# Optimization experiments

Hardware: AMD Instinct MI355X
Metric: run time of the kernel (lower is better)

## Reference

```python
import jax, jax.numpy as jnp
import numpy as np

H, DH = 12, 64
D = H * DH
EPS = 1e-5
NEG = -10000.0


def _layernorm(x, gamma, beta):
    mu = jnp.mean(x, axis=-1, keepdims=True)
    var = jnp.mean(jnp.square(x - mu), axis=-1, keepdims=True)
    return (x - mu) * jax.lax.rsqrt(var + EPS) * gamma + beta


def setup_inputs() -> dict:
    key = jax.random.key(0)
    ks = jax.random.split(key, 10)
    B, E, L = 1, 64, 256
    x = jax.random.normal(ks[0], (B, E, L, D), dtype=jnp.float32)
    padding_mask = jax.random.bernoulli(ks[1], 0.1, (B, E, L))
    s = 1.0 / np.sqrt(D)
    w_row = jax.random.normal(ks[2], (3 * D, D), dtype=jnp.float32) * s
    b_row = jnp.zeros((3 * D,), dtype=jnp.float32)
    w_col = jax.random.normal(ks[3], (3 * D, D), dtype=jnp.float32) * s
    b_col = jnp.zeros((3 * D,), dtype=jnp.float32)
    gamma1 = jnp.ones((D,), dtype=jnp.float32)
    beta1 = jnp.zeros((D,), dtype=jnp.float32)
    gamma2 = jnp.ones((D,), dtype=jnp.float32)
    beta2 = jnp.zeros((D,), dtype=jnp.float32)
    return {"x": x, "padding_mask": padding_mask, "w_row": w_row, "b_row": b_row,
            "w_col": w_col, "b_col": b_col, "gamma1": gamma1, "beta1": beta1,
            "gamma2": gamma2, "beta2": beta2}


def _qkv(x, w, b, B, E, L):
    qkv = x @ w.T + b  # [B,E,L,3D]
    q, k, v = jnp.split(qkv, 3, axis=-1)
    rs = lambda t: t.reshape(B, E, L, H, DH)
    return rs(q), rs(k), rs(v)


def reference(x, padding_mask, w_row, b_row, w_col, b_col, gamma1, beta1, gamma2, beta2):
    B, E, L, _ = x.shape
    mask = jnp.where(padding_mask, NEG, 0.0).astype(x.dtype)  # [B,E,L], same per head

    # ---- tied row attention ----
    q, k, v = _qkv(x, w_row, b_row, B, E, L)
    q = q * (DH * E) ** (-0.5)
    row_logits = jnp.einsum('bsihc,bsjhc->bhij', q, k)  # [B,H,L,L], tied over E
    row_logits = row_logits + mask.sum(axis=1)[:, None, None, :]  # sum over E, bcast over i,h
    row_maps = jax.nn.softmax(row_logits, axis=-1)
    row_out = jnp.einsum('bhij,bsjhc->bsihc', row_maps, v).reshape(B, E, L, D)
    out = _layernorm(x + row_out, gamma1, beta1)

    # ---- column attention ----
    q, k, v = _qkv(out, w_col, b_col, B, E, L)
    q = q * DH ** (-0.5)
    col_logits = jnp.einsum('bilhc,bjlhc->bhijl', q, k)  # [B,H,E,E,L]
    col_logits = col_logits + mask[:, None, None, :, :]  # bcast over h,i; applied along j
    col_maps = jax.nn.softmax(col_logits, axis=-2)
    col_out = jnp.einsum('bhijl,bjlhc->bilhc', col_maps, v).reshape(B, E, L, D)
    out = _layernorm(out + col_out, gamma2, beta2)

    return out, row_maps[:, :, None, :, :]  # row maps returned as [B,H,1,L,L]
```

## Files before the change

### kernel.cpp

```cpp
#include <hip/hip_runtime.h>
#include <hip/hip_bf16.h>
#include <float.h>

#define E_  64
#define L_  256
#define D_  768
#define H_  12
#define DH_ 64
#define TD_ 2304
#define NEGV -10000.0f
#define EPS_ 1e-5f

#define GM 16384
#define GN 2304
#define GK 768

#define RSPLIT 8

typedef __attribute__((ext_vector_type(8))) __bf16 bf16x8;
typedef __attribute__((ext_vector_type(4))) float f32x4;
typedef __attribute__((ext_vector_type(8))) unsigned short u16x8;

__device__ __forceinline__ float wred_sum64(float v){
  #pragma unroll
  for (int o = 32; o > 0; o >>= 1) v += __shfl_xor(v, o, 64);
  return v;
}
__device__ __forceinline__ float wred_max64(float v){
  #pragma unroll
  for (int o = 32; o > 0; o >>= 1) v = fmaxf(v, __shfl_xor(v, o, 64));
  return v;
}
__device__ __forceinline__ unsigned short f2bf(float f){
  unsigned int u = __float_as_uint(f);
  u += 0x7FFF + ((u >> 16) & 1);
  return (unsigned short)(u >> 16);
}
__device__ __forceinline__ float bf2f(unsigned short s){
  return __uint_as_float(((unsigned int)s) << 16);
}

__global__ __launch_bounds__(256) void f2b_kernel(
    const float* __restrict__ in, unsigned short* __restrict__ out){
  size_t i = ((size_t)blockIdx.x * 256 + threadIdx.x) * 8;
  float4 a = *(const float4*)(in + i);
  float4 b = *(const float4*)(in + i + 4);
  u16x8 o;
  o[0]=f2bf(a.x); o[1]=f2bf(a.y); o[2]=f2bf(a.z); o[3]=f2bf(a.w);
  o[4]=f2bf(b.x); o[5]=f2bf(b.y); o[6]=f2bf(b.z); o[7]=f2bf(b.w);
  *(u16x8*)(out + i) = o;
}

__global__ void masksum_kernel(const int* __restrict__ pm, float* __restrict__ msum){
  int l = threadIdx.x;
  int cnt = 0;
  #pragma unroll
  for (int s = 0; s < E_; ++s) cnt += (pm[s * L_ + l] != 0);
  msum[l] = NEGV * (float)cnt;
}

__global__ __launch_bounds__(256) void gemm_mfma_nt(
    const unsigned short* __restrict__ A,
    const unsigned short* __restrict__ W,
    const float* __restrict__ bias,
    unsigned short* __restrict__ C){
  __shared__ unsigned short As[128*32] __attribute__((aligned(16)));
  __shared__ unsigned short Bs[128*32] __attribute__((aligned(16)));
  int tid = threadIdx.x;
  int lane = tid & 63, wave = tid >> 6;
  int wr = wave >> 1, wc = wave & 1;
  int m0 = blockIdx.y * 128, n0 = blockIdx.x * 128;
  int col16 = lane & 15, kgrp = lane >> 4;

  f32x4 zero = {0.f, 0.f, 0.f, 0.f};
  f32x4 acc[4][4];
  #pragma unroll
  for (int mf = 0; mf < 4; ++mf)
    #pragma unroll
    for (int nf = 0; nf < 4; ++nf) acc[mf][nf] = zero;

  int srow = lane >> 2;
  int kchunk = (lane & 3) * 8;
  const unsigned short* Ag = A + (size_t)(m0 + wave * 32 + srow) * GK + kchunk;
  const unsigned short* Wg = W + (size_t)(n0 + wave * 32 + srow) * GK + kchunk;
  unsigned short* AsB = &As[(wave * 32) * 32];
  unsigned short* BsB = &Bs[(wave * 32) * 32];

  for (int k0 = 0; k0 < GK; k0 += 32) {
    __syncthreads();
    __builtin_amdgcn_global_load_lds(
      (const __attribute__((address_space(1))) unsigned int*)(Ag + k0),
      (__attribute__((address_space(3))) unsigned int*)(AsB), 16, 0, 0);
    __builtin_amdgcn_global_load_lds(
      (const __attribute__((address_space(1))) unsigned int*)(Ag + 16 * GK + k0),
      (__attribute__((address_space(3))) unsigned int*)(AsB + 16 * 32), 16, 0, 0);
    __builtin_amdgcn_global_load_lds(
      (const __attribute__((address_space(1))) unsigned int*)(Wg + k0),
      (__attribute__((address_space(3))) unsigned int*)(BsB), 16, 0, 0);
    __builtin_amdgcn_global_load_lds(
      (const __attribute__((address_space(1))) unsigned int*)(Wg + 16 * GK + k0),
      (__attribute__((address_space(3))) unsigned int*)(BsB + 16 * 32), 16, 0, 0);
    __syncthreads();
    bf16x8 af[4], bfr[4];
    #pragma unroll
    for (int mf = 0; mf < 4; ++mf)
      af[mf] = *(const bf16x8*)&As[(wr * 64 + mf * 16 + col16) * 32 + kgrp * 8];
    #pragma unroll
    for (int nf = 0; nf < 4; ++nf)
      bfr[nf] = *(const bf16x8*)&Bs[(wc * 64 + nf * 16 + col16) * 32 + kgrp * 8];
    #pragma unroll
    for (int mf = 0; mf < 4; ++mf)
      #pragma unroll
      for (int nf = 0; nf < 4; ++nf)
        acc[mf][nf] = __builtin_amdgcn_mfma_f32_16x16x32_bf16(af[mf], bfr[nf], acc[mf][nf], 0, 0, 0);
  }

  float bv[4];
  #pragma unroll
  for (int nf = 0; nf < 4; ++nf) bv[nf] = bias[n0 + wc * 64 + nf * 16 + col16];
  #pragma unroll
  for (int mf = 0; mf < 4; ++mf){
    int rbase = m0 + wr * 64 + mf * 16 + kgrp * 4;
    #pragma unroll
    for (int j = 0; j < 4; ++j){
      unsigned short* crow = C + (size_t)(rbase + j) * GN + n0 + wc * 64 + col16;
      #pragma unroll
      for (int nf = 0; nf < 4; ++nf)
        crow[nf * 16] = f2bf(acc[mf][nf][j] + bv[nf]);
    }
  }
}

__global__ __launch_bounds__(256) void row_logits_mfma(
    const unsigned short* __restrict__ qkvb, float* __restrict__ rlogp){
  __shared__ unsigned short As[128*64] __attribute__((aligned(16)));
  __shared__ unsigned short Bs[128*64] __attribute__((aligned(16)));
  int p = blockIdx.x;
  int tile = blockIdx.y;
  int h = blockIdx.z;
  int i0 = (tile >> 1) * 128, j0 = (tile & 1) * 128;
  int tid = threadIdx.x;
  int lane = tid & 63, wave = tid >> 6;
  int wr = wave >> 1, wc = wave & 1;
  int lanelow = lane & 15, kgrp = lane >> 4;

  f32x4 zero = {0.f, 0.f, 0.f, 0.f};
  f32x4 acc[4][4];
  #pragma unroll
  for (int mf = 0; mf < 4; ++mf)
    #pragma unroll
    for (int nf = 0; nf < 4; ++nf) acc[mf][nf] = zero;

  int cb8 = tid & 7;
  const unsigned short* qb = qkvb + h * DH_;
  const unsigned short* kb = qkvb + D_ + h * DH_;

  for (int ss = 0; ss < E_ / RSPLIT; ++ss){
    int s = p * (E_ / RSPLIT) + ss;
    size_t sb = (size_t)s * L_ * TD_;
    __syncthreads();
    #pragma unroll
    for (int q = 0; q < 4; ++q){
      int row = q * 32 + (tid >> 3);
      int srcoff = (cb8 * 8) ^ ((row & 7) * 8);
      unsigned short* ldsA = &As[(q * 256 + wave * 64) * 8];
      unsigned short* ldsB = &Bs[(q * 256 + wave * 64) * 8];
      __builtin_amdgcn_global_load_lds(
        (const __attribute__((address_space(1))) unsigned int*)(qb + sb + (size_t)(i0 + row) * TD_ + srcoff),
        (__attribute__((address_space(3))) unsigned int*)ldsA, 16, 0, 0);
      __builtin_amdgcn_global_load_lds(
        (const __attribute__((address_space(1))) unsigned int*)(kb + sb + (size_t)(j0 + row) * TD_ + srcoff),
        (__attribute__((address_space(3))) unsigned int*)ldsB, 16, 0, 0);
    }
    __syncthreads();
    #pragma unroll
    for (int c0 = 0; c0 < 64; c0 += 32){
      bf16x8 af[4], bfr[4];
      #pragma unroll
      for (int mf = 0; mf < 4; ++mf){
        int row = wr * 64 + mf * 16 + lanelow;
        af[mf] = *(const bf16x8*)&As[row * 64 + ((c0 + kgrp * 8) ^ ((row & 7) * 8))];
      }
      #pragma unroll
      for (int nf = 0; nf < 4; ++nf){
        int row = wc * 64 + nf * 16 + lanelow;
        bfr[nf] = *(const bf16x8*)&Bs[row * 64 + ((c0 + kgrp * 8) ^ ((row & 7) * 8))];
      }
      #pragma unroll
      for (int mf = 0; mf < 4; ++mf)
        #pragma unroll
        for (int nf = 0; nf < 4; ++nf)
          acc[mf][nf] = __builtin_amdgcn_mfma_f32_16x16x32_bf16(af[mf], bfr[nf], acc[mf][nf], 0, 0, 0);
    }
  }

  float* outp = rlogp + ((size_t)p * H_ + h) * (L_ * L_);
  #pragma unroll
  for (int mf = 0; mf < 4; ++mf){
    int ibase = i0 + wr * 64 + mf * 16 + kgrp * 4;
    #pragma unroll
    for (int j2 = 0; j2 < 4; ++j2){
      float* orow = outp + (size_t)(ibase + j2) * L_ + j0 + wc * 64 + lanelow;
      #pragma unroll
      for (int nf = 0; nf < 4; ++nf)
        orow[nf * 16] = acc[mf][nf][j2];
    }
  }
}

__global__ __launch_bounds__(256) void row_softmax_kernel(
    const float* __restrict__ rlogp, const float* __restrict__ msum,
    float* __restrict__ maps, unsigned short* __restrict__ mapsb){
  int row = blockIdx.x;
  int t = threadIdx.x;
  float v = 0.f;
  #pragma unroll
  for (int pp = 0; pp < RSPLIT; ++pp)
    v += rlogp[(size_t)pp * (H_ * L_ * L_) + (size_t)row * L_ + t];
  v = v * (1.0f / 64.0f) + msum[t];
  __shared__ float red[8];
  float m = wred_max64(v);
  int wid = t >> 6;
  if ((t & 63) == 0) red[wid] = m;
  __syncthreads();
  float bm = fmaxf(fmaxf(red[0], red[1]), fmaxf(red[2], red[3]));
  float e = __expf(v - bm);
  float s = wred_sum64(e);
  if ((t & 63) == 0) red[4 + wid] = s;
  __syncthreads();
  float bs = (red[4] + red[5]) + (red[6] + red[7]);
  float p = e / bs;
  maps[(size_t)row * L_ + t] = p;
  mapsb[(size_t)row * L_ + t] = f2bf(p);
}

__global__ __launch_bounds__(256) void vtrans_kernel(
    const unsigned short* __restrict__ qkvb, unsigned short* __restrict__ vt){
  __shared__ unsigned short T[64 * 265];
  int s = blockIdx.x, h = blockIdx.y;
  int t = threadIdx.x;
  const unsigned short* vb = qkvb + 2 * D_ + h * DH_;
  int jr = t >> 3, c0 = (t & 7) * 8;
  #pragma unroll
  for (int pass = 0; pass < 8; ++pass){
    int j = pass * 32 + jr;
    u16x8 r = *(const u16x8*)(vb + ((size_t)s * L_ + j) * TD_ + c0);
    #pragma unroll
    for (int e = 0; e < 8; ++e) T[(c0 + e) * 265 + j] = r[e];
  }
  __syncthreads();
  unsigned short* ob = vt + ((size_t)(s * H_ + h) * DH_) * L_;
  int c = t >> 2;
  #pragma unroll
  for (int u = 0; u < 8; ++u){
    int j0 = ((t & 3) + u * 4) * 8;
    u16x8 w;
    #pragma unroll
    for (int e = 0; e < 8; ++e) w[e] = T[c * 265 + j0 + e];
    *(u16x8*)(ob + (size_t)c * L_ + j0) = w;
  }
}

__global__ __launch_bounds__(256) void row_pv_mfma(
    const unsigned short* __restrict__ mapsb, const unsigned short* __restrict__ vt,
    const float* __restrict__ x, unsigned short* __restrict__ rowtmp){
  __shared__ unsigned short As[256*32] __attribute__((aligned(16)));
  __shared__ unsigned short Bs[64*32] __attribute__((aligned(16)));
  int s = blockIdx.x, h = blockIdx.y;
  int tid = threadIdx.x;
  int lane = tid & 63, wave = tid >> 6;
  int lanelow = lane & 15, kgrp = lane >> 4;

  f32x4 zero = {0.f, 0.f, 0.f, 0.f};
  f32x4 acc[4][4];
  #pragma unroll
  for (int mf = 0; mf < 4; ++mf)
    #pragma unroll
    for (int nf = 0; nf < 4; ++nf) acc[mf][nf] = zero;

  int srow = lane >> 2;
  int kchunk = (lane & 3) * 8;
  const unsigned short* Ag = mapsb + (size_t)h * (L_ * L_) + (size_t)(wave * 64 + srow) * L_ + kchunk;
  const unsigned short* Bg = vt + (((size_t)s * H_ + h) * DH_ + wave * 16 + srow) * L_ + kchunk;
  unsigned short* AsB = &As[(wave * 64) * 32];
  unsigned short* BsB = &Bs[(wave * 16) * 32];

  for (int k0 = 0; k0 < L_; k0 += 32){
    __syncthreads();
    #pragma unroll
    for (int u = 0; u < 4; ++u)
      __builtin_amdgcn_global_load_lds(
        (const __attribute__((address_space(1))) unsigned int*)(Ag + (size_t)u * 16 * L_ + k0),
        (__attribute__((address_space(3))) unsigned int*)(AsB + u * 16 * 32), 16, 0, 0);
    __builtin_amdgcn_global_load_lds(
      (const __attribute__((address_space(1))) unsigned int*)(Bg + k0),
      (__attribute__((address_space(3))) unsigned int*)(BsB), 16, 0, 0);
    __syncthreads();
    bf16x8 af[4], bfr[4];
    #pragma unroll
    for (int mf = 0; mf < 4; ++mf)
      af[mf] = *(const bf16x8*)&As[(wave * 64 + mf * 16 + lanelow) * 32 + kgrp * 8];
    #pragma unroll
    for (int nf = 0; nf < 4; ++nf)
      bfr[nf] = *(const bf16x8*)&Bs[(nf * 16 + lanelow) * 32 + kgrp * 8];
    #pragma unroll
    for (int mf = 0; mf < 4; ++mf)
      #pragma unroll
      for (int nf = 0; nf < 4; ++nf)
        acc[mf][nf] = __builtin_amdgcn_mfma_f32_16x16x32_bf16(af[mf], bfr[nf], acc[mf][nf], 0, 0, 0);
  }

  #pragma unroll
  for (int mf = 0; mf < 4; ++mf){
    int ibase = wave * 64 + mf * 16 + kgrp * 4;
    #pragma unroll
    for (int j2 = 0; j2 < 4; ++j2){
      size_t rb = ((size_t)s * L_ + ibase + j2) * D_ + h * DH_ + lanelow;
      #pragma unroll
      for (int nf = 0; nf < 4; ++nf)
        rowtmp[rb + nf * 16] = f2bf(acc[mf][nf][j2] + x[rb + nf * 16]);
    }
  }
}

__global__ __launch_bounds__(256) void ln1_kernel(
    const unsigned short* __restrict__ a,
    const float* __restrict__ g, const float* __restrict__ be,
    unsigned short* __restrict__ outb){
  int row = blockIdx.x;
  int t = threadIdx.x;
  const unsigned short* pa = a + (size_t)row * D_;
  float v[3];
  float s1 = 0.f, s2 = 0.f;
  #pragma unroll
  for (int u = 0; u < 3; ++u){
    int c = t + u * 256;
    float xv = bf2f(pa[c]);
    v[u] = xv; s1 += xv; s2 += xv * xv;
  }
  s1 = wred_sum64(s1); s2 = wred_sum64(s2);
  __shared__ float red[8];
  int wid = t >> 6;
  if ((t & 63) == 0){ red[wid] = s1; red[4 + wid] = s2; }
  __syncthreads();
  float ts1 = (red[0] + red[1]) + (red[2] + red[3]);
  float ts2 = (red[4] + red[5]) + (red[6] + red[7]);
  float mu = ts1 * (1.0f / D_);
  float var = ts2 * (1.0f / D_) - mu * mu;
  float rs = rsqrtf(var + EPS_);
  #pragma unroll
  for (int u = 0; u < 3; ++u){
    int c = t + u * 256;
    outb[(size_t)row * D_ + c] = f2bf((v[u] - mu) * rs * g[c] + be[c]);
  }
}

__global__ __launch_bounds__(256) void ln2_kernel(
    const unsigned short* __restrict__ ab,
    const unsigned short* __restrict__ b,
    const float* __restrict__ g, const float* __restrict__ be,
    float* __restrict__ out){
  int row = blockIdx.x;
  int t = threadIdx.x;
  const unsigned short* pa = ab + (size_t)row * D_;
  const unsigned short* pb = b + (size_t)row * D_;
  float v[3];
  float s1 = 0.f, s2 = 0.f;
  #pragma unroll
  for (int u = 0; u < 3; ++u){
    int c = t + u * 256;
    float xv = bf2f(pa[c]) + bf2f(pb[c]);
    v[u] = xv; s1 += xv; s2 += xv * xv;
  }
  s1 = wred_sum64(s1); s2 = wred_sum64(s2);
  __shared__ float red[8];
  int wid = t >> 6;
  if ((t & 63) == 0){ red[wid] = s1; red[4 + wid] = s2; }
  __syncthreads();
  float ts1 = (red[0] + red[1]) + (red[2] + red[3]);
  float ts2 = (red[4] + red[5]) + (red[6] + red[7]);
  float mu = ts1 * (1.0f / D_);
  float var = ts2 * (1.0f / D_) - mu * mu;
  float rs = rsqrtf(var + EPS_);
  #pragma unroll
  for (int u = 0; u < 3; ++u){
    int c = t + u * 256;
    out[(size_t)row * D_ + c] = (v[u] - mu) * rs * g[c] + be[c];
  }
}

__global__ __launch_bounds__(256) void col_attn_mfma(
    const unsigned short* __restrict__ qkvb, const int* __restrict__ pm,
    unsigned short* __restrict__ colout){
  __shared__ unsigned short Qs[64*64] __attribute__((aligned(16)));
  __shared__ unsigned short Ks[64*64] __attribute__((aligned(16)));
  __shared__ unsigned short Vt[64*64] __attribute__((aligned(16)));
  __shared__ unsigned short Ps[64*64] __attribute__((aligned(16)));
  __shared__ float cmask[64];
  int l = blockIdx.x, h = blockIdx.y;
  int tid = threadIdx.x;
  int lane = tid & 63, wave = tid >> 6;
  int lanelow = lane & 15, kgrp = lane >> 4;

  const unsigned short* qb = qkvb + h * DH_;
  const unsigned short* kb = qkvb + D_ + h * DH_;
  const unsigned short* vb = qkvb + 2 * D_ + h * DH_;

  if (tid < 64) cmask[tid] = (pm[tid * L_ + l] != 0) ? NEGV : 0.f;

  {
    int row = tid >> 3, ch = tid & 7;
    #pragma unroll
    for (int pass = 0; pass < 2; ++pass){
      int r2 = row + pass * 32;
      size_t gbase = ((size_t)r2 * L_ + l) * TD_ + ch * 8;
      u16x8 q8 = *(const u16x8*)(qb + gbase);
      u16x8 k8 = *(const u16x8*)(kb + gbase);
      int dst = r2 * 64 + ((ch ^ (r2 & 7)) * 8);
      *(u16x8*)&Qs[dst] = q8;
      *(u16x8*)&Ks[dst] = k8;
    }
  }
  {
    int jr = tid & 31, ch = tid >> 5;
    #pragma unroll
    for (int pass = 0; pass < 2; ++pass){
      int j = jr + pass * 32;
      u16x8 v8 = *(const u16x8*)(vb + ((size_t)j * L_ + l) * TD_ + ch * 8);
      #pragma unroll
      for (int e = 0; e < 8; ++e){
        int c = ch * 8 + e;
        Vt[c * 64 + (((j >> 3) ^ (c & 7)) * 8) + (j & 7)] = v8[e];
      }
    }
  }
  __syncthreads();

  f32x4 zero = {0.f, 0.f, 0.f, 0.f};
  f32x4 acc[4] = {zero, zero, zero, zero};
  int irow = wave * 16 + lanelow;
  #pragma unroll
  for (int ks = 0; ks < 2; ++ks){
    bf16x8 af = *(const bf16x8*)&Qs[irow * 64 + (((ks * 4 + kgrp) ^ (irow & 7)) * 8)];
    #pragma unroll
    for (int nf = 0; nf < 4; ++nf){
      int jrow = nf * 16 + lanelow;
      bf16x8 bk = *(const bf16x8*)&Ks[jrow * 64 + (((ks * 4 + kgrp) ^ (jrow & 7)) * 8)];
      acc[nf] = __builtin_amdgcn_mfma_f32_16x16x32_bf16(af, bk, acc[nf], 0, 0, 0);
    }
  }
  float cm[4];
  #pragma unroll
  for (int nf = 0; nf < 4; ++nf) cm[nf] = cmask[nf * 16 + lanelow];
  #pragma unroll
  for (int r = 0; r < 4; ++r){
    float pvv[4];
    float m = -FLT_MAX;
    #pragma unroll
    for (int nf = 0; nf < 4; ++nf){
      pvv[nf] = acc[nf][r] * 0.125f + cm[nf];
      m = fmaxf(m, pvv[nf]);
    }
    m = fmaxf(m, __shfl_xor(m, 1, 64));
    m = fmaxf(m, __shfl_xor(m, 2, 64));
    m = fmaxf(m, __shfl_xor(m, 4, 64));
    m = fmaxf(m, __shfl_xor(m, 8, 64));
    float s = 0.f;
    #pragma unroll
    for (int nf = 0; nf < 4; ++nf){ pvv[nf] = __expf(pvv[nf] - m); s += pvv[nf]; }
    s += __shfl_xor(s, 1, 64);
    s += __shfl_xor(s, 2, 64);
    s += __shfl_xor(s, 4, 64);
    s += __shfl_xor(s, 8, 64);
    float inv = 1.0f / s;
    int i = wave * 16 + kgrp * 4 + r;
    #pragma unroll
    for (int nf = 0; nf < 4; ++nf){
      int j = nf * 16 + lanelow;
      Ps[i * 64 + (((j >> 3) ^ (i & 7)) * 8) + (j & 7)] = f2bf(pvv[nf] * inv);
    }
  }
  __syncthreads();

  f32x4 acc2[4] = {zero, zero, zero, zero};
  #pragma unroll
  for (int ks = 0; ks < 2; ++ks){
    bf16x8 pa = *(const bf16x8*)&Ps[irow * 64 + (((ks * 4 + kgrp) ^ (irow & 7)) * 8)];
    #pragma unroll
    for (int nf = 0; nf < 4; ++nf){
      int crow = nf * 16 + lanelow;
      bf16x8 bv = *(const bf16x8*)&Vt[crow * 64 + (((ks * 4 + kgrp) ^ (crow & 7)) * 8)];
      acc2[nf] = __builtin_amdgcn_mfma_f32_16x16x32_bf16(pa, bv, acc2[nf], 0, 0, 0);
    }
  }
  #pragma unroll
  for (int r = 0; r < 4; ++r){
    int i = wave * 16 + kgrp * 4 + r;
    size_t ob = ((size_t)i * L_ + l) * D_ + h * DH_ + lanelow;
    #pragma unroll
    for (int nf = 0; nf < 4; ++nf)
      colout[ob + nf * 16] = f2bf(acc2[nf][r]);
  }
}

extern "C" void kernel_launch(void* const* d_in, const int* in_sizes, int n_in,
                              void* d_out, int out_size, void* d_ws, size_t ws_size,
                              hipStream_t stream){
  (void)in_sizes; (void)n_in; (void)out_size; (void)ws_size;
  const float* x     = (const float*)d_in[0];
  const int*   pm    = (const int*)  d_in[1];
  const float* w_row = (const float*)d_in[2];
  const float* b_row = (const float*)d_in[3];
  const float* w_col = (const float*)d_in[4];
  const float* b_col = (const float*)d_in[5];
  const float* g1    = (const float*)d_in[6];
  const float* be1   = (const float*)d_in[7];
  const float* g2    = (const float*)d_in[8];
  const float* be2   = (const float*)d_in[9];

  float* out  = (float*)d_out;
  float* maps = out + (size_t)E_ * L_ * D_;

  float* F    = (float*)d_ws;
  unsigned short* qkvb = (unsigned short*)F;
  unsigned short* tmpb16 = (unsigned short*)(F + 18874368);
  unsigned short* out1b = (unsigned short*)(F + 31457280);
  float* msum = F + 37748736;
  float* rlogp = F + 37748992;
  unsigned short* wrb = (unsigned short*)(F + 44040448);
  unsigned short* wcb = (unsigned short*)(F + 44925184);
  unsigned short* mapsb = (unsigned short*)(F + 45809920);
  unsigned short* vtb = (unsigned short*)(F + 46203136);

  const int M = E_ * L_;
  const int NX = M * D_;
  const int NW = TD_ * D_;

  masksum_kernel<<<1, 256, 0, stream>>>(pm, msum);
  f2b_kernel<<<NX / 2048, 256, 0, stream>>>(x, tmpb16);
  f2b_kernel<<<NW / 2048, 256, 0, stream>>>(w_row, wrb);
  f2b_kernel<<<NW / 2048, 256, 0, stream>>>(w_col, wcb);

  gemm_mfma_nt<<<dim3(GN/128, GM/128), 256, 0, stream>>>(tmpb16, wrb, b_row, qkvb);
  vtrans_kernel<<<dim3(E_, H_), 256, 0, stream>>>(qkvb, vtb);
  row_logits_mfma<<<dim3(RSPLIT, 4, H_), 256, 0, stream>>>(qkvb, rlogp);
  row_softmax_kernel<<<H_ * L_, 256, 0, stream>>>(rlogp, msum, maps, mapsb);
  row_pv_mfma<<<dim3(E_, H_), 256, 0, stream>>>(mapsb, vtb, x, tmpb16);
  ln1_kernel<<<M, 256, 0, stream>>>(tmpb16, g1, be1, out1b);
  gemm_mfma_nt<<<dim3(GN/128, GM/128), 256, 0, stream>>>(out1b, wcb, b_col, qkvb);
  col_attn_mfma<<<dim3(L_, H_), 256, 0, stream>>>(qkvb, pm, tmpb16);
  ln2_kernel<<<M, 256, 0, stream>>>(out1b, tmpb16, g2, be2, out);
}
```

Baseline: 288.0 us.

## Deepen GEMM K-tile to 64 with XOR-swizzled LDS and XCD-aware block remap

The QKV projection GEMM now stages 64-wide K tiles instead of 32, which halves the number of barrier pairs per output tile. LDS rows are stored with an XOR swizzle of 8-element chunks to avoid bank conflicts when reading MFMA fragments. The 2D grid becomes a 1D grid whose block index is remapped, so that consecutive blocks placed on the same XCD cover neighbouring tiles and share cache. LDS use doubles and there is still no double buffering, so global-load latency stays exposed each iteration.

Result: slower. 294.8 us (+2.3%).

```diff
diff --git a/kernel.cpp b/kernel.cpp
--- a/kernel.cpp
+++ b/kernel.cpp
@@ -16,6 +16,7 @@
 #define GK 768
 
 #define RSPLIT 8
+#define NWG_GEMM ((GN/128)*(GM/128))
 
 typedef __attribute__((ext_vector_type(8))) __bf16 bf16x8;
 typedef __attribute__((ext_vector_type(4))) float f32x4;
@@ -64,13 +65,16 @@
     const unsigned short* __restrict__ W,
     const float* __restrict__ bias,
     unsigned short* __restrict__ C){
-  __shared__ unsigned short As[128*32] __attribute__((aligned(16)));
-  __shared__ unsigned short Bs[128*32] __attribute__((aligned(16)));
+  __shared__ unsigned short As[128*64] __attribute__((aligned(16)));
+  __shared__ unsigned short Bs[128*64] __attribute__((aligned(16)));
+  int lin = blockIdx.x;
+  int swz = (lin & 7) * (NWG_GEMM / 8) + (lin >> 3);
+  int m0 = (swz / (GN/128)) * 128;
+  int n0 = (swz % (GN/128)) * 128;
   int tid = threadIdx.x;
   int lane = tid & 63, wave = tid >> 6;
   int wr = wave >> 1, wc = wave & 1;
-  int m0 = blockIdx.y * 128, n0 = blockIdx.x * 128;
-  int col16 = lane & 15, kgrp = lane >> 4;
+  int lanelow = lane & 15, kgrp = lane >> 4;
 
   f32x4 zero = {0.f, 0.f, 0.f, 0.f};
   f32x4 acc[4][4];
@@ -79,51 +83,56 @@
     #pragma unroll
     for (int nf = 0; nf < 4; ++nf) acc[mf][nf] = zero;
 
-  int srow = lane >> 2;
-  int kchunk = (lane & 3) * 8;
-  const unsigned short* Ag = A + (size_t)(m0 + wave * 32 + srow) * GK + kchunk;
-  const unsigned short* Wg = W + (size_t)(n0 + wave * 32 + srow) * GK + kchunk;
-  unsigned short* AsB = &As[(wave * 32) * 32];
-  unsigned short* BsB = &Bs[(wave * 32) * 32];
-
-  for (int k0 = 0; k0 < GK; k0 += 32) {
+  int cb8 = tid & 7;
+  int strow = tid >> 3;
+
+  for (int kt = 0; kt < GK / 64; ++kt){
+    int k0 = kt * 64;
     __syncthreads();
-    __builtin_amdgcn_global_load_lds(
-      (const __attribute__((address_space(1))) unsigned int*)(Ag + k0),
-      (__attribute__((address_space(3))) unsigned int*)(AsB), 16, 0, 0);
-    __builtin_amdgcn_global_load_lds(
-      (const __attribute__((address_space(1))) unsigned int*)(Ag + 16 * GK + k0),
-      (__attribute__((address_space(3))) unsigned int*)(AsB + 16 * 32), 16, 0, 0);
-    __builtin_amdgcn_global_load_lds(
-      (const __attribute__((address_space(1))) unsigned int*)(Wg + k0),
-      (__attribute__((address_space(3))) unsigned int*)(BsB), 16, 0, 0);
-    __builtin_amdgcn_global_load_lds(
-      (const __attribute__((address_space(1))) unsigned int*)(Wg + 16 * GK + k0),
-      (__attribute__((address_space(3))) unsigned int*)(BsB + 16 * 32), 16, 0, 0);
+    #pragma unroll
+    for (int q = 0; q < 4; ++q){
+      int row = q * 32 + strow;
+      int srcoff = (cb8 * 8) ^ ((row & 7) * 8);
+      unsigned short* ldsA = &As[(q * 256 + wave * 64) * 8];
+      unsigned short* ldsB = &Bs[(q * 256 + wave * 64) * 8];
+      __builtin_amdgcn_global_load_lds(
+        (const __attribute__((address_space(1))) unsigned int*)(A + (size_t)(m0 + row) * GK + k0 + srcoff),
+        (__attribute__((address_space(3))) unsigned int*)ldsA, 16, 0, 0);
+      __builtin_amdgcn_global_load_lds(
+        (const __attribute__((address_space(1))) unsigned int*)(W + (size_t)(n0 + row) * GK + k0 + srcoff),
+        (__attribute__((address_space(3))) unsigned int*)ldsB, 16, 0, 0);
+    }
     __syncthreads();
-    bf16x8 af[4], bfr[4];
-    #pragma unroll
-    for (int mf = 0; mf < 4; ++mf)
-      af[mf] = *(const bf16x8*)&As[(wr * 64 + mf * 16 + col16) * 32 + kgrp * 8];
-    #pragma unroll
-    for (int nf = 0; nf < 4; ++nf)
-      bfr[nf] = *(const bf16x8*)&Bs[(wc * 64 + nf * 16 + col16) * 32 + kgrp * 8];
-    #pragma unroll
-    for (int mf = 0; mf < 4; ++mf)
-      #pragma unroll
-      for (int nf = 0; nf < 4; ++nf)
-        acc[mf][nf] = __builtin_amdgcn_mfma_f32_16x16x32_bf16(af[mf], bfr[nf], acc[mf][nf], 0, 0, 0);
+    #pragma unroll
+    for (int c0 = 0; c0 < 64; c0 += 32){
+      bf16x8 af[4], bfr[4];
+      #pragma unroll
+      for (int mf = 0; mf < 4; ++mf){
+        int row = wr * 64 + mf * 16 + lanelow;
+        af[mf] = *(const bf16x8*)&As[row * 64 + ((c0 + kgrp * 8) ^ ((row & 7) * 8))];
+      }
+      #pragma unroll
+      for (int nf = 0; nf < 4; ++nf){
+        int row = wc * 64 + nf * 16 + lanelow;
+        bfr[nf] = *(const bf16x8*)&Bs[row * 64 + ((c0 + kgrp * 8) ^ ((row & 7) * 8))];
+      }
+      #pragma unroll
+      for (int mf = 0; mf < 4; ++mf)
+        #pragma unroll
+        for (int nf = 0; nf < 4; ++nf)
+          acc[mf][nf] = __builtin_amdgcn_mfma_f32_16x16x32_bf16(af[mf], bfr[nf], acc[mf][nf], 0, 0, 0);
+    }
   }
 
   float bv[4];
   #pragma unroll
-  for (int nf = 0; nf < 4; ++nf) bv[nf] = bias[n0 + wc * 64 + nf * 16 + col16];
+  for (int nf = 0; nf < 4; ++nf) bv[nf] = bias[n0 + wc * 64 + nf * 16 + lanelow];
   #pragma unroll
   for (int mf = 0; mf < 4; ++mf){
     int rbase = m0 + wr * 64 + mf * 16 + kgrp * 4;
     #pragma unroll
     for (int j = 0; j < 4; ++j){
-      unsigned short* crow = C + (size_t)(rbase + j) * GN + n0 + wc * 64 + col16;
+      unsigned short* crow = C + (size_t)(rbase + j) * GN + n0 + wc * 64 + lanelow;
       #pragma unroll
       for (int nf = 0; nf < 4; ++nf)
         crow[nf * 16] = f2bf(acc[mf][nf][j] + bv[nf]);
@@ -541,13 +550,13 @@
   f2b_kernel<<<NW / 2048, 256, 0, stream>>>(w_row, wrb);
   f2b_kernel<<<NW / 2048, 256, 0, stream>>>(w_col, wcb);
 
-  gemm_mfma_nt<<<dim3(GN/128, GM/128), 256, 0, stream>>>(tmpb16, wrb, b_row, qkvb);
+  gemm_mfma_nt<<<NWG_GEMM, 256, 0, stream>>>(tmpb16, wrb, b_row, qkvb);
   vtrans_kernel<<<dim3(E_, H_), 256, 0, stream>>>(qkvb, vtb);
   row_logits_mfma<<<dim3(RSPLIT, 4, H_), 256, 0, stream>>>(qkvb, rlogp);
   row_softmax_kernel<<<H_ * L_, 256, 0, stream>>>(rlogp, msum, maps, mapsb);
   row_pv_mfma<<<dim3(E_, H_), 256, 0, stream>>>(mapsb, vtb, x, tmpb16);
   ln1_kernel<<<M, 256, 0, stream>>>(tmpb16, g1, be1, out1b);
-  gemm_mfma_nt<<<dim3(GN/128, GM/128), 256, 0, stream>>>(out1b, wcb, b_col, qkvb);
+  gemm_mfma_nt<<<NWG_GEMM, 256, 0, stream>>>(out1b, wcb, b_col, qkvb);
   col_attn_mfma<<<dim3(L_, H_), 256, 0, stream>>>(qkvb, pm, tmpb16);
   ln2_kernel<<<M, 256, 0, stream>>>(out1b, tmpb16, g2, be2, out);
 }
```
